# Performance work log

Measured on AMD Instinct MI355X. Metric: run time of the kernel, lower is better.

The kernel has to match this reference:

```python
import jax, jax.numpy as jnp
import numpy as np

LMAX = 4  # number of l blocks (lmax+1 in the original)
# segment ids mapping the L2 = sum(2l+1) = 16 spherical components to their l block
SEG = np.repeat(np.arange(LMAX), 2 * np.arange(LMAX) + 1)  # [16]
SEG_ONEHOT = np.eye(LMAX, dtype=np.float32)[SEG]  # [16, LMAX]


def setup_inputs() -> dict:
    key = jax.random.key(0)
    ks = jax.random.split(key, 10)
    b, m, f, k, L2 = 16, 64, 128, 64, 16
    def rnd(kk, shape, scale):
        return jax.random.normal(kk, shape, dtype=jnp.float32) * scale
    return {
        'x': rnd(ks[0], (b, m, f, L2), 1.0),
        'y': rnd(ks[1], (b, m, f, L2), 1.0),
        'wx0': rnd(ks[2], (k, f, f, LMAX), 1.0 / np.sqrt(f * f * LMAX)),
        'wy0': rnd(ks[3], (k, f, f, LMAX), 1.0 / np.sqrt(f * f * LMAX)),
        'wx_mlp': rnd(ks[4], (2, k, k), 1.0 / np.sqrt(k)),
        'bx_mlp': rnd(ks[5], (2, k, k), 0.02),
        'wy_mlp': rnd(ks[6], (2, k, k), 1.0 / np.sqrt(k)),
        'by_mlp': rnd(ks[7], (2, k, k), 0.02),
        'wxf': rnd(ks[8], (LMAX, f, k), 1.0 / np.sqrt(k)),
        'wyf': rnd(ks[9], (LMAX, f, k), 1.0 / np.sqrt(k)),
    }


def reference(x, y, wx0, wy0, wx_mlp, bx_mlp, wy_mlp, by_mlp, wxf, wyf):
    act = jax.nn.silu
    S = jnp.asarray(SEG_ONEHOT)  # [L2, lmax]
    # outer product of y and x features, segment-summed over each l block:
    # mix[b,m,fy,fx,l] = sum_c y[b,m,fy,c] * x[b,m,fx,c] * S[c,l]
    mix = jnp.einsum('bmfc,bmgc,cl->bmfgl', y, x, S)  # [b,m,f,f,lmax]
    mx = jnp.einsum('bmfgl,kfgl->bmk', mix, wx0)
    my = jnp.einsum('bmfgl,kfgl->bmk', mix, wy0)
    for i in range(wx_mlp.shape[0]):  # the n_mlp-1 used MLP stages
        mx = act(jnp.einsum('bmk,kl->bml', mx, wx_mlp[i]) + bx_mlp[i])
        my = act(jnp.einsum('bmk,kl->bml', my, wy_mlp[i]) + by_mlp[i])
    mx = act(jnp.einsum('bmk,lfk->bmfl', mx, wxf))  # [b,m,f,lmax]
    my = act(jnp.einsum('bmk,lfk->bmfl', my, wyf))
    # broadcast each l gate over its 2l+1 components (repeat == gather by SEG)
    seg = jnp.asarray(SEG)
    res = mx[..., seg] * x + my[..., seg] * y  # [b,m,f,L2]
    return res
```

## Files before the change

kernel.cpp:

```cpp
#include <hip/hip_runtime.h>
#include <stdint.h>


#define AS1 __attribute__((address_space(1)))
#define AS3 __attribute__((address_space(3)))

typedef __bf16 bf16x8 __attribute__((ext_vector_type(8)));
typedef float f32x4 __attribute__((ext_vector_type(4)));

__device__ __forceinline__ uint16_t f2b(float f) {
  uint32_t u = __float_as_uint(f);
  u += 0x7fffu + ((u >> 16) & 1u);
  return (uint16_t)(u >> 16);
}

#if __has_builtin(__builtin_amdgcn_fdot2_f32_bf16)
typedef __bf16 bf16x2 __attribute__((ext_vector_type(2)));
__device__ __forceinline__ float dot2b(uint32_t a, uint32_t b, float c) {
  union { uint32_t u; bf16x2 v; } ua, ub;
  ua.u = a; ub.u = b;
  return __builtin_amdgcn_fdot2_f32_bf16(ua.v, ub.v, c, false);
}
#else
__device__ __forceinline__ float dot2b(uint32_t a, uint32_t b, float c) {
  float a0 = __uint_as_float(a << 16), a1 = __uint_as_float(a & 0xffff0000u);
  float b0 = __uint_as_float(b << 16), b1 = __uint_as_float(b & 0xffff0000u);
  return c + a0 * b0 + a1 * b1;
}
#endif

__global__ __launch_bounds__(256) void convert_all(
    const float* __restrict__ wx0, const float* __restrict__ wy0,
    const float* __restrict__ x, const float* __restrict__ y,
    const float* __restrict__ wxf, const float* __restrict__ wyf,
    uint16_t* __restrict__ Wb, uint16_t* __restrict__ xb,
    uint16_t* __restrict__ yb, float* __restrict__ wfT) {
  if (blockIdx.x >= 6144) {
    int base = (blockIdx.x - 6144) * 2048 + threadIdx.x * 8;
#pragma unroll
    for (int ii = 0; ii < 8; ++ii) {
      int idx = base + ii;
      int side = idx >> 15, rem = idx & 32767;
      int k = rem >> 9, l = (rem >> 7) & 3, f = rem & 127;
      const float* src = side ? wyf : wxf;
      wfT[idx] = src[((size_t)l * 128 + f) * 64 + k];
    }
    return;
  }
  size_t i = ((size_t)blockIdx.x * 256 + threadIdx.x) * 8;
  const float* s; uint16_t* d;
  if (i < 4194304)        { s = wx0 + i;              d = Wb + i; }
  else if (i < 8388608)   { s = wy0 + (i - 4194304);  d = Wb + i; }
  else if (i < 10485760)  { s = x + (i - 8388608);    d = xb + (i - 8388608); }
  else                    { s = y + (i - 10485760);   d = yb + (i - 10485760); }
  float4 v0 = *(const float4*)s;
  float4 v1 = *(const float4*)(s + 4);
  uint32_t o0 = (uint32_t)f2b(v0.x) | ((uint32_t)f2b(v0.y) << 16);
  uint32_t o1 = (uint32_t)f2b(v0.z) | ((uint32_t)f2b(v0.w) << 16);
  uint32_t o2 = (uint32_t)f2b(v1.x) | ((uint32_t)f2b(v1.y) << 16);
  uint32_t o3 = (uint32_t)f2b(v1.z) | ((uint32_t)f2b(v1.w) << 16);
  *(uint4*)d = make_uint4(o0, o1, o2, o3);
}

__device__ __forceinline__ void gload_lds16(const void* g, void* l) {
  __builtin_amdgcn_global_load_lds((const AS1 uint32_t*)g, (AS3 uint32_t*)l, 16, 0, 0);
}

__global__ __launch_bounds__(256, 3) void fused_gemm(
    const uint16_t* __restrict__ xb, const uint16_t* __restrict__ yb,
    const uint16_t* __restrict__ Wb, float* __restrict__ Cpart) {
  __shared__ __align__(16) uint16_t sA[2][128 * 40];
  __shared__ __align__(16) uint16_t sB[2][128 * 32];
  __shared__ __align__(16) uint16_t yS[2][2048];

  int tid = threadIdx.x;
  int w = tid >> 6, lane = tid & 63;
  int g_id = blockIdx.x;
  int fb = g_id >> 3, fyg = g_id & 7;
  int FB = fb * 8;
  int fy0 = fyg * 16;
  int m0 = blockIdx.y * 128;
  int r = lane & 15, q = lane >> 4;
  int wm = w >> 1, wn = w & 1;
  int rowl = lane >> 2, qq = lane & 3;
  int m_loc = tid & 127, half = tid >> 7;

  uint32_t xr[32];
  {
    const uint16_t* xp0 = xb + (size_t)(m0 + m_loc) * 2048 + (FB + half * 4) * 16;
#pragma unroll
    for (int j = 0; j < 8; ++j) {
      uint4 v = *(const uint4*)(xp0 + j * 8);
      xr[j * 4 + 0] = v.x; xr[j * 4 + 1] = v.y;
      xr[j * 4 + 2] = v.z; xr[j * 4 + 3] = v.w;
    }
  }

  f32x4 zero = {0.f, 0.f, 0.f, 0.f};
  f32x4 acc[4][4];
#pragma unroll
  for (int i = 0; i < 4; ++i)
#pragma unroll
    for (int j = 0; j < 4; ++j) acc[i][j] = zero;

  int bcol = qq ^ ((rowl >> 1) & 3);
  int ychunk = w >> 1, ymbase = (w & 1) * 64;
  const uint16_t* ysrc_base = yb + (size_t)(m0 + ymbase + lane) * 2048 + ychunk * 8;
  int ydst_off = ychunk * 1024 + ymbase * 8;

  auto issueB = [&](uint16_t* dstB, int t) {
    int kk0 = (fy0 + t) * 512 + FB * 4;
#pragma unroll
    for (int jj = 0; jj < 2; ++jj) {
      int blk = w * 2 + jj;
      int rowi = blk * 16 + rowl;
      gload_lds16(Wb + (size_t)rowi * 65536 + kk0 + bcol * 8, dstB + blk * 512);
    }
  };
  auto issueY = [&](uint16_t* dstY, int t) {
    gload_lds16(ysrc_base + (size_t)(fy0 + t) * 16, dstY + ydst_off);
  };
  auto computeG = [&](const uint16_t* srcY, float* gg) {
    uint4 ya = *(const uint4*)(srcY + m_loc * 8);
    uint4 yc = *(const uint4*)(srcY + 1024 + m_loc * 8);
    uint32_t yp[8] = {ya.x, ya.y, ya.z, ya.w, yc.x, yc.y, yc.z, yc.w};
    uint32_t yl0 = yp[0] & 0xffffu, yh0 = yp[0] & 0xffff0000u;
    uint32_t yl4 = yp[4] & 0xffffu, yh4 = yp[4] & 0xffff0000u;
#pragma unroll
    for (int fxp = 0; fxp < 4; ++fxp) {
      const uint32_t* xp = xr + fxp * 8;
      gg[fxp * 4 + 0] = dot2b(xp[0], yl0, 0.f);
      gg[fxp * 4 + 1] = dot2b(xp[1], yp[1], dot2b(xp[0], yh0, 0.f));
      gg[fxp * 4 + 2] = dot2b(xp[4], yl4,
                         dot2b(xp[3], yp[3], dot2b(xp[2], yp[2], 0.f)));
      gg[fxp * 4 + 3] = dot2b(xp[7], yp[7], dot2b(xp[6], yp[6],
                         dot2b(xp[5], yp[5], dot2b(xp[4], yh4, 0.f))));
    }
  };
  auto writeA = [&](uint16_t* dstA, const float* gg) {
    uint32_t o[8];
#pragma unroll
    for (int p = 0; p < 8; ++p)
      o[p] = (__float_as_uint(gg[2 * p]) >> 16) |
             (__float_as_uint(gg[2 * p + 1]) & 0xffff0000u);
    uint16_t* dst = dstA + m_loc * 40 + half * 16;
    *(uint4*)dst       = make_uint4(o[0], o[1], o[2], o[3]);
    *(uint4*)(dst + 8) = make_uint4(o[4], o[5], o[6], o[7]);
  };

  uint16_t *pAc = sA[0], *pAn = sA[1];
  uint16_t *pBc = sB[0], *pBn = sB[1];
  uint16_t *pYc = yS[0], *pYn = yS[1];

  float gg[16];
  issueY(pYc, 0);
  __syncthreads();
  computeG(pYc, gg);
  writeA(pAc, gg);
  issueB(pBc, 0);
  issueY(pYn, 1);
  __syncthreads();

  for (int t = 0; t < 16; ++t) {
    if (t < 15) {
      issueB(pBn, t + 1);
      if (t < 14) issueY(pYc, t + 2);
      computeG(pYn, gg);
      writeA(pAn, gg);
    }
    bf16x8 a[4], b[4];
#pragma unroll
    for (int i = 0; i < 4; ++i)
      a[i] = *(const bf16x8*)&pAc[(wm * 64 + i * 16 + r) * 40 + q * 8];
#pragma unroll
    for (int j = 0; j < 4; ++j) {
      int row = wn * 64 + j * 16 + r;
      int pos = q ^ ((row >> 1) & 3);
      b[j] = *(const bf16x8*)&pBc[row * 32 + pos * 8];
    }
#pragma unroll
    for (int i = 0; i < 4; ++i)
#pragma unroll
      for (int j = 0; j < 4; ++j)
        acc[i][j] = __builtin_amdgcn_mfma_f32_16x16x32_bf16(a[i], b[j], acc[i][j], 0, 0, 0);
    __syncthreads();
    uint16_t* tp;
    tp = pAc; pAc = pAn; pAn = tp;
    tp = pBc; pBc = pBn; pBn = tp;
    tp = pYc; pYc = pYn; pYn = tp;
  }

  float* cbase = Cpart + (size_t)g_id * 131072;
#pragma unroll
  for (int i = 0; i < 4; ++i)
#pragma unroll
    for (int j = 0; j < 4; ++j)
#pragma unroll
      for (int reg = 0; reg < 4; ++reg) {
        int mm = m0 + wm * 64 + i * 16 + q * 4 + reg;
        int nn = wn * 64 + j * 16 + r;
        cbase[(size_t)mm * 128 + nn] = acc[i][j][reg];
      }
}

__global__ __launch_bounds__(256) void reduce_kernel(
    const float* __restrict__ Cpart, float* __restrict__ Cred) {
  __shared__ float sred[256];
  int t = threadIdx.x, bm = blockIdx.x;
  int col = t & 127, hh = t >> 7;
  float s = 0.f;
#pragma unroll 8
  for (int sp = hh * 64; sp < hh * 64 + 64; ++sp)
    s += Cpart[(size_t)sp * 131072 + (size_t)bm * 128 + col];
  sred[t] = s;
  __syncthreads();
  if (t < 128) Cred[(size_t)bm * 128 + t] = sred[t] + sred[t + 128];
}

__global__ __launch_bounds__(256) void finish_kernel(
    const float* __restrict__ x, const float* __restrict__ y,
    const float* __restrict__ wx_mlp, const float* __restrict__ bx_mlp,
    const float* __restrict__ wy_mlp, const float* __restrict__ by_mlp,
    const float* __restrict__ wfT,
    const float* __restrict__ Cred, float* __restrict__ out) {
  const int seg[16] = {0,1,1,1,2,2,2,2,2,3,3,3,3,3,3,3};
  __shared__ float sm[128];
  __shared__ float sg[2][128][4];
  int t = threadIdx.x;
  int bm = blockIdx.x;
  int mi = bm & 63;

  if (t < 128) sm[t] = Cred[(size_t)bm * 128 + t];
  __syncthreads();

  for (int st = 0; st < 2; ++st) {
    float v = 0.f;
    if (t < 128) {
      int side = t >> 6, j = t & 63;
      const float* wmlp = side ? wy_mlp : wx_mlp;
      const float* bmlp = side ? by_mlp : bx_mlp;
      const float* mv = sm + side * 64;
#pragma unroll 8
      for (int k = 0; k < 64; ++k)
        v += mv[k] * wmlp[(st * 64 + k) * 64 + j];
      v += bmlp[(st * 64 + mi) * 64 + j];
      v = v / (1.f + __expf(-v));
    }
    __syncthreads();
    if (t < 128) sm[t] = v;
    __syncthreads();
  }

  {
    int side = t >> 7, f = t & 127;
    const float* base = wfT + side * 32768;
    const float* mv = sm + side * 64;
    float gg[4] = {0.f, 0.f, 0.f, 0.f};
#pragma unroll 8
    for (int k = 0; k < 64; ++k) {
      float m2 = mv[k];
#pragma unroll
      for (int l = 0; l < 4; ++l)
        gg[l] += m2 * base[(k * 4 + l) * 128 + f];
    }
#pragma unroll
    for (int l = 0; l < 4; ++l)
      sg[side][f][l] = gg[l] / (1.f + __expf(-gg[l]));
  }
  __syncthreads();

  {
    int f = t >> 1, half = t & 1;
    size_t base = ((size_t)bm * 128 + f) * 16 + half * 8;
    float4 xa = *(const float4*)(x + base), xb4 = *(const float4*)(x + base + 4);
    float4 ya = *(const float4*)(y + base), yb4 = *(const float4*)(y + base + 4);
    float xv[8] = {xa.x, xa.y, xa.z, xa.w, xb4.x, xb4.y, xb4.z, xb4.w};
    float yv[8] = {ya.x, ya.y, ya.z, ya.w, yb4.x, yb4.y, yb4.z, yb4.w};
    float o[8];
#pragma unroll
    for (int ii = 0; ii < 8; ++ii) {
      int c = half * 8 + ii;
      o[ii] = sg[0][f][seg[c]] * xv[ii] + sg[1][f][seg[c]] * yv[ii];
    }
    *(float4*)(out + base)     = make_float4(o[0], o[1], o[2], o[3]);
    *(float4*)(out + base + 4) = make_float4(o[4], o[5], o[6], o[7]);
  }
}

extern "C" void kernel_launch(void* const* d_in, const int* in_sizes, int n_in,
                              void* d_out, int out_size, void* d_ws, size_t ws_size,
                              hipStream_t stream) {
  const float* x      = (const float*)d_in[0];
  const float* y      = (const float*)d_in[1];
  const float* wx0    = (const float*)d_in[2];
  const float* wy0    = (const float*)d_in[3];
  const float* wx_mlp = (const float*)d_in[4];
  const float* bx_mlp = (const float*)d_in[5];
  const float* wy_mlp = (const float*)d_in[6];
  const float* by_mlp = (const float*)d_in[7];
  const float* wxf    = (const float*)d_in[8];
  const float* wyf    = (const float*)d_in[9];
  float* out = (float*)d_out;

  uint16_t* Wb    = (uint16_t*)d_ws;
  uint16_t* xb    = (uint16_t*)((char*)d_ws + (size_t)16777216);
  uint16_t* yb    = (uint16_t*)((char*)d_ws + (size_t)20971520);
  float*    Cpart = (float*)((char*)d_ws + (size_t)25165824);
  float*    wfT   = (float*)((char*)d_ws + (size_t)92274688);
  float*    Cred  = (float*)((char*)d_ws + (size_t)92536832);

  convert_all<<<6176, 256, 0, stream>>>(wx0, wy0, x, y, wxf, wyf, Wb, xb, yb, wfT);
  fused_gemm<<<dim3(128, 8), 256, 0, stream>>>(xb, yb, Wb, Cpart);
  reduce_kernel<<<1024, 256, 0, stream>>>(Cpart, Cred);
  finish_kernel<<<1024, 256, 0, stream>>>(x, y, wx_mlp, bx_mlp, wy_mlp, by_mlp,
                                          wfT, Cred, out);
}
```

Baseline: 182.5 us.

## Halve split-K partials, triple-buffer GEMM pipeline, fold reduction into finish kernel

Each GEMM block now covers 32 fy rows instead of 16, which halves the grid and the number of split-K partial tiles written to global memory. The main loop becomes a three-stage buffer ring for B and y, waited on with explicit vmcnt barriers rather than full syncthreads, and the MFMA section is wrapped in raised wave priority. The separate reduce kernel is removed; the finish kernel now sums the 64 partials itself, saving one launch and one round trip through global memory. The cost is more LDS per block, an occupancy bound lowered to 2 blocks per SIMD set, and fewer blocks to spread across the CUs.

```diff
diff --git a/kernel.cpp b/kernel.cpp
--- a/kernel.cpp
+++ b/kernel.cpp
@@ -66,19 +66,22 @@
   __builtin_amdgcn_global_load_lds((const AS1 uint32_t*)g, (AS3 uint32_t*)l, 16, 0, 0);
 }
 
-__global__ __launch_bounds__(256, 3) void fused_gemm(
+#define PIPE_BAR(N) \
+  asm volatile("s_waitcnt vmcnt(" #N ") lgkmcnt(0)\n\ts_barrier" ::: "memory")
+
+__global__ __launch_bounds__(256, 2) void fused_gemm(
     const uint16_t* __restrict__ xb, const uint16_t* __restrict__ yb,
     const uint16_t* __restrict__ Wb, float* __restrict__ Cpart) {
   __shared__ __align__(16) uint16_t sA[2][128 * 40];
-  __shared__ __align__(16) uint16_t sB[2][128 * 32];
-  __shared__ __align__(16) uint16_t yS[2][2048];
+  __shared__ __align__(16) uint16_t sB[3][128 * 32];
+  __shared__ __align__(16) uint16_t yS[3][2048];
 
   int tid = threadIdx.x;
   int w = tid >> 6, lane = tid & 63;
   int g_id = blockIdx.x;
-  int fb = g_id >> 3, fyg = g_id & 7;
+  int fb = g_id >> 2, fyg = g_id & 3;
   int FB = fb * 8;
-  int fy0 = fyg * 16;
+  int fy0 = fyg * 32;
   int m0 = blockIdx.y * 128;
   int r = lane & 15, q = lane >> 4;
   int wm = w >> 1, wn = w & 1;
@@ -148,26 +151,25 @@
     *(uint4*)(dst + 8) = make_uint4(o[4], o[5], o[6], o[7]);
   };
 
+  float gg[16];
+  issueY(yS[0], 0);
+  __syncthreads();
+  computeG(yS[0], gg);
+  writeA(sA[0], gg);
+  issueB(sB[0], 0);
+  issueY(yS[1], 1);
+  issueB(sB[1], 1);
+  issueY(yS[2], 2);
+  PIPE_BAR(3);
+
   uint16_t *pAc = sA[0], *pAn = sA[1];
-  uint16_t *pBc = sB[0], *pBn = sB[1];
-  uint16_t *pYc = yS[0], *pYn = yS[1];
-
-  float gg[16];
-  issueY(pYc, 0);
-  __syncthreads();
-  computeG(pYc, gg);
-  writeA(pAc, gg);
-  issueB(pBc, 0);
-  issueY(pYn, 1);
-  __syncthreads();
-
-  for (int t = 0; t < 16; ++t) {
-    if (t < 15) {
-      issueB(pBn, t + 1);
-      if (t < 14) issueY(pYc, t + 2);
-      computeG(pYn, gg);
-      writeA(pAn, gg);
-    }
+  uint16_t *pBread = sB[0], *pBmid = sB[1], *pBissue = sB[2];
+  uint16_t *pYcomp = yS[1], *pYmid = yS[2], *pYissue = yS[0];
+
+  for (int t = 0; t < 32; ++t) {
+    if (t <= 29) issueB(pBissue, t + 2);
+    if (t <= 28) issueY(pYissue, t + 3);
+
     bf16x8 a[4], b[4];
 #pragma unroll
     for (int i = 0; i < 4; ++i)
@@ -176,18 +178,30 @@
     for (int j = 0; j < 4; ++j) {
       int row = wn * 64 + j * 16 + r;
       int pos = q ^ ((row >> 1) & 3);
-      b[j] = *(const bf16x8*)&pBc[row * 32 + pos * 8];
-    }
+      b[j] = *(const bf16x8*)&pBread[row * 32 + pos * 8];
+    }
+
+    if (t < 31) {
+      computeG(pYcomp, gg);
+      writeA(pAn, gg);
+    }
+
+    __builtin_amdgcn_s_setprio(1);
 #pragma unroll
     for (int i = 0; i < 4; ++i)
 #pragma unroll
       for (int j = 0; j < 4; ++j)
         acc[i][j] = __builtin_amdgcn_mfma_f32_16x16x32_bf16(a[i], b[j], acc[i][j], 0, 0, 0);
-    __syncthreads();
+    __builtin_amdgcn_s_setprio(0);
+
+    if (t <= 28)      PIPE_BAR(3);
+    else if (t == 29) PIPE_BAR(2);
+    else if (t == 30) PIPE_BAR(0);
+
     uint16_t* tp;
     tp = pAc; pAc = pAn; pAn = tp;
-    tp = pBc; pBc = pBn; pBn = tp;
-    tp = pYc; pYc = pYn; pYn = tp;
+    tp = pBread; pBread = pBmid; pBmid = pBissue; pBissue = tp;
+    tp = pYcomp; pYcomp = pYmid; pYmid = pYissue; pYissue = tp;
   }
 
   float* cbase = Cpart + (size_t)g_id * 131072;
@@ -203,34 +217,31 @@
       }
 }
 
-__global__ __launch_bounds__(256) void reduce_kernel(
-    const float* __restrict__ Cpart, float* __restrict__ Cred) {
-  __shared__ float sred[256];
-  int t = threadIdx.x, bm = blockIdx.x;
-  int col = t & 127, hh = t >> 7;
-  float s = 0.f;
-#pragma unroll 8
-  for (int sp = hh * 64; sp < hh * 64 + 64; ++sp)
-    s += Cpart[(size_t)sp * 131072 + (size_t)bm * 128 + col];
-  sred[t] = s;
-  __syncthreads();
-  if (t < 128) Cred[(size_t)bm * 128 + t] = sred[t] + sred[t + 128];
-}
-
 __global__ __launch_bounds__(256) void finish_kernel(
     const float* __restrict__ x, const float* __restrict__ y,
     const float* __restrict__ wx_mlp, const float* __restrict__ bx_mlp,
     const float* __restrict__ wy_mlp, const float* __restrict__ by_mlp,
     const float* __restrict__ wfT,
-    const float* __restrict__ Cred, float* __restrict__ out) {
+    const float* __restrict__ Cpart, float* __restrict__ out) {
   const int seg[16] = {0,1,1,1,2,2,2,2,2,3,3,3,3,3,3,3};
+  __shared__ float sred[256];
   __shared__ float sm[128];
   __shared__ float sg[2][128][4];
   int t = threadIdx.x;
   int bm = blockIdx.x;
   int mi = bm & 63;
 
-  if (t < 128) sm[t] = Cred[(size_t)bm * 128 + t];
+  {
+    int col = t & 127, hh = t >> 7;
+    const float* cp = Cpart + (size_t)(hh * 32) * 131072 + (size_t)bm * 128 + col;
+    float s = 0.f;
+#pragma unroll 8
+    for (int sp = 0; sp < 32; ++sp)
+      s += cp[(size_t)sp * 131072];
+    sred[t] = s;
+  }
+  __syncthreads();
+  if (t < 128) sm[t] = sred[t] + sred[t + 128];
   __syncthreads();
 
   for (int st = 0; st < 2; ++st) {
@@ -306,12 +317,10 @@
   uint16_t* xb    = (uint16_t*)((char*)d_ws + (size_t)16777216);
   uint16_t* yb    = (uint16_t*)((char*)d_ws + (size_t)20971520);
   float*    Cpart = (float*)((char*)d_ws + (size_t)25165824);
-  float*    wfT   = (float*)((char*)d_ws + (size_t)92274688);
-  float*    Cred  = (float*)((char*)d_ws + (size_t)92536832);
+  float*    wfT   = (float*)((char*)d_ws + (size_t)58720256);
 
   convert_all<<<6176, 256, 0, stream>>>(wx0, wy0, x, y, wxf, wyf, Wb, xb, yb, wfT);
-  fused_gemm<<<dim3(128, 8), 256, 0, stream>>>(xb, yb, Wb, Cpart);
-  reduce_kernel<<<1024, 256, 0, stream>>>(Cpart, Cred);
+  fused_gemm<<<dim3(64, 8), 256, 0, stream>>>(xb, yb, Wb, Cpart);
   finish_kernel<<<1024, 256, 0, stream>>>(x, y, wx_mlp, bx_mlp, wy_mlp, by_mlp,
-                                          wfT, Cred, out);
-}
+                                          wfT, Cpart, out);
+}
```

After: 169.4 us. -7.2%, faster.
